# Kernel optimization log

Measured on AMD Instinct MI355X. Metric: run time of the kernel, lower is better.

## Reference

```python
import jax, jax.numpy as jnp
import numpy as np

B, N, S, K = 16, 4, 64, 50        # batch, n_answers, q_len, n_boxes
VD, QD, H = 1024, 768, 512        # v_dim, q_dim, num_hid


def setup_inputs() -> dict:
    key = jax.random.key(0)
    ks = jax.random.split(key, 10)
    inp = {
        "v": jax.random.normal(ks[0], (B, 1, K, VD), dtype=jnp.float32),
        "q": jax.random.normal(ks[1], (B, N, S, 1, QD), dtype=jnp.float32),
        "box_mask": jax.random.randint(ks[2], (B, K), 0, 2, dtype=jnp.int32),
        "tags_attention": jax.random.normal(ks[3], (B, K), dtype=jnp.float32),
        # learned params (nn.Linear stores weight as [out, in])
        "Wv": jax.random.normal(ks[4], (H, VD), dtype=jnp.float32) * 0.02,
        "bv": jnp.zeros((H,), dtype=jnp.float32),
        "Wq": jax.random.normal(ks[5], (H, QD), dtype=jnp.float32) * 0.02,
        "bq": jnp.zeros((H,), dtype=jnp.float32),
        "Wl": jax.random.normal(ks[6], (1, H), dtype=jnp.float32) * 0.02,
        "bl": jnp.zeros((1,), dtype=jnp.float32),
    }
    return inp


def reference(v, q, box_mask, tags_attention, Wv, bv, Wq, bq, Wl, bl):
    # v_proj = Linear(v).unsqueeze(1): [B,1,K,H] -> [B,1,1,K,H]
    v_proj = (jnp.einsum('bokd,hd->bokh', v, Wv) + bv)[:, None]
    # q_proj: [B,N,S,1,H]
    q_proj = jnp.einsum('bnsod,hd->bnsoh', q, Wq) + bq
    # broadcast add + tanh: joint_repr [B,N,S,K,H] (the big intermediate)
    joint_repr = jnp.tanh(v_proj + q_proj)
    # score reduce over H: logits [B,N,S,K]
    logits = jnp.einsum('bnskh,oh->bnsko', joint_repr, Wl)[..., 0] + bl[0]
    # masked softmax over boxes with mask box_mask[:,None,None] -> [B,1,1,K]
    mask = (box_mask > 0)[:, None, None]
    w = jax.nn.softmax(jnp.where(mask, logits, jnp.float32(-1e9)), axis=-1)
    return w
```

## Files before the change

kernel.cpp:

```cpp
#include <hip/hip_runtime.h>
#include <hip/hip_bf16.h>
#include <cstddef>


typedef __attribute__((ext_vector_type(4))) float        f32x4;
typedef __attribute__((ext_vector_type(8))) short        bfrag;
typedef __attribute__((ext_vector_type(4))) unsigned int u32x4;

__device__ __forceinline__ void gload4(const float* g, float* l) {
  __builtin_amdgcn_global_load_lds((const __attribute__((address_space(1))) void*)g,
                                   (__attribute__((address_space(3))) void*)l, 4, 0, 0);
}

__device__ __forceinline__ unsigned int cvtpk(float a, float b) {
  unsigned int r;
  asm("v_cvt_pk_bf16_f32 %0, %1, %2" : "=v"(r) : "v"(a), "v"(b));
  return r;
}

__global__ void __launch_bounds__(256) gemm_fused(
    const float* __restrict__ v,  const float* __restrict__ q,
    const float* __restrict__ Wv, const float* __restrict__ bv,
    const float* __restrict__ Wq, const float* __restrict__ bq,
    float* __restrict__ vpw, float* __restrict__ qpw) {
  __shared__ unsigned short As[2][64 * 64];
  __shared__ unsigned short Bs[2][64 * 64];

  const int id = blockIdx.x;
  const int m  = (id & 7) + ((id >> 6) << 3);
  const int nt = (id >> 3) & 7;
  if (m >= 77) return;

  const int t = threadIdx.x;

  const float* A; const float* W; const float* bias; float* C;
  int M, Kd, m0;
  if (m < 13) { A = v; W = Wv; bias = bv; C = vpw; M = 800;  Kd = 1024; m0 = m * 64; }
  else        { A = q; W = Wq; bias = bq; C = qpw; M = 4096; Kd = 768;  m0 = (m - 13) * 64; }
  const int n0 = nt * 64;

  const int lane = t & 63;
  const int wave = t >> 6;
  const int wm   = wave >> 1;
  const int wn   = wave & 1;
  const int la   = lane & 15;
  const int lb   = lane >> 4;

  const int srow = t >> 2;
  const int skq  = (t & 3) * 16;

  int gr = m0 + srow; if (gr >= M) gr = M - 1;
  const float* Arow = A + (size_t)gr * Kd + skq;
  const float* Wrow = W + (size_t)(n0 + srow) * Kd + skq;

  f32x4 acc[2][2] = {};
  f32x4 raA[4], rbA[4], raB[4], rbB[4];

  auto loadG = [&](f32x4* ra, f32x4* rb, int s) {
    const float* ap = Arow + s * 64;
    const float* wp = Wrow + s * 64;
#pragma unroll
    for (int i = 0; i < 4; ++i) ra[i] = *(const f32x4*)&ap[i * 4];
#pragma unroll
    for (int i = 0; i < 4; ++i) rb[i] = *(const f32x4*)&wp[i * 4];
  };

  const int o0 = (srow * 128 + skq * 2)      ^ ((srow & 7) << 4);
  const int o1 = (srow * 128 + skq * 2 + 16) ^ ((srow & 7) << 4);

  auto writeL = [&](unsigned short* da, unsigned short* db,
                    const f32x4* ra, const f32x4* rb) {
    u32x4 p;
    p[0] = cvtpk(ra[0][0], ra[0][1]); p[1] = cvtpk(ra[0][2], ra[0][3]);
    p[2] = cvtpk(ra[1][0], ra[1][1]); p[3] = cvtpk(ra[1][2], ra[1][3]);
    *(u32x4*)((char*)da + o0) = p;
    p[0] = cvtpk(ra[2][0], ra[2][1]); p[1] = cvtpk(ra[2][2], ra[2][3]);
    p[2] = cvtpk(ra[3][0], ra[3][1]); p[3] = cvtpk(ra[3][2], ra[3][3]);
    *(u32x4*)((char*)da + o1) = p;
    p[0] = cvtpk(rb[0][0], rb[0][1]); p[1] = cvtpk(rb[0][2], rb[0][3]);
    p[2] = cvtpk(rb[1][0], rb[1][1]); p[3] = cvtpk(rb[1][2], rb[1][3]);
    *(u32x4*)((char*)db + o0) = p;
    p[0] = cvtpk(rb[2][0], rb[2][1]); p[1] = cvtpk(rb[2][2], rb[2][3]);
    p[2] = cvtpk(rb[3][0], rb[3][1]); p[3] = cvtpk(rb[3][2], rb[3][3]);
    *(u32x4*)((char*)db + o1) = p;
  };

  auto compute = [&](const unsigned short* sa, const unsigned short* sb) {
    bfrag af[2][2], bf[2][2];
#pragma unroll
    for (int r = 0; r < 2; ++r)
#pragma unroll
      for (int kk = 0; kk < 2; ++kk) {
        int rowa = wm * 32 + r * 16 + la;
        af[r][kk] = *(const bfrag*)((const char*)sa +
                     ((rowa * 128 + kk * 64 + lb * 16) ^ ((rowa & 7) << 4)));
        int rowb = wn * 32 + r * 16 + la;
        bf[r][kk] = *(const bfrag*)((const char*)sb +
                     ((rowb * 128 + kk * 64 + lb * 16) ^ ((rowb & 7) << 4)));
      }
#pragma unroll
    for (int kk = 0; kk < 2; ++kk)
#pragma unroll
      for (int r = 0; r < 2; ++r)
#pragma unroll
        for (int c = 0; c < 2; ++c)
          acc[r][c] = __builtin_amdgcn_mfma_f32_16x16x32_bf16(af[r][kk], bf[c][kk], acc[r][c], 0, 0, 0);
  };

  const int nsteps = Kd >> 6;
  loadG(raA, rbA, 0);
  writeL(As[0], Bs[0], raA, rbA);
  loadG(raB, rbB, 1);
  __syncthreads();
  for (int s = 0; s < nsteps; s += 2) {
    if (s + 2 < nsteps) loadG(raA, rbA, s + 2);
    compute(As[0], Bs[0]);
    writeL(As[1], Bs[1], raB, rbB);
    __syncthreads();
    if (s + 3 < nsteps) loadG(raB, rbB, s + 3);
    compute(As[1], Bs[1]);
    if (s + 2 < nsteps) writeL(As[0], Bs[0], raA, rbA);
    __syncthreads();
  }

  const float CEXP = 2.885390081777927f;
#pragma unroll
  for (int c = 0; c < 2; ++c) {
    int col = n0 + wn * 32 + c * 16 + la;
    float bcol = bias[col];
#pragma unroll
    for (int r = 0; r < 2; ++r) {
      int mbase = m0 + wm * 32 + r * 16 + lb * 4;
#pragma unroll
      for (int e = 0; e < 4; ++e) {
        int mr = mbase + e;
        if (mr < M)
          C[(size_t)mr * 512 + col] =
              __builtin_amdgcn_exp2f((acc[r][c][e] + bcol) * CEXP);
      }
    }
  }
}

__global__ void __launch_bounds__(512) stage3_kernel(
    const float* __restrict__ vp, const float* __restrict__ qp,
    const float* __restrict__ wl, const int* __restrict__ box_mask,
    float* __restrict__ out) {
  __shared__ float vpS[2][50][64];
  __shared__ float qpS[2][8][64];
  __shared__ float wlS[2][64];

  const int b     = blockIdx.y;
  const int chunk = blockIdx.x;
  const int t     = threadIdx.x;
  const int wv    = t >> 6;
  const int k     = t & 63;
  const int rowg  = b * 256 + chunk * 8 + wv;
  const float* qrow = qp + (size_t)rowg * 512;

  const int kc = (k < 50) ? k : k - 14;
  const int cb = kc * 256 + ((kc & 7) << 4);
  const int lsrc = k ^ (wv << 2);

  auto STAGE = [&](int buf, int h0) {
#pragma unroll
    for (int i = 0; i < 7; ++i) {
      int kr = i * 8 + wv;
      if (kr < 50)
        gload4(vp + (size_t)(b * 50 + kr) * 512 + h0 + lsrc, &vpS[buf][kr][0]);
    }
    gload4(qrow + h0 + k, &qpS[buf][wv][0]);
    if (wv == 0) gload4(wl + h0 + k, &wlS[buf][0]);
  };

  float a0 = 0.f, a1 = 0.f, a2 = 0.f, a3 = 0.f;

  STAGE(0, 0);
  __syncthreads();
  int buf = 0;
  for (int c = 0; c < 8; ++c) {
    if (c < 7) STAGE(buf ^ 1, (c + 1) * 64);
    const char* vb = (const char*)&vpS[buf][0][0];
#pragma unroll
    for (int hh = 0; hh < 64; hh += 4) {
      f32x4 v4 = *(const f32x4*)(vb + (cb ^ (hh << 2)));
      f32x4 q4 = *(const f32x4*)&qpS[buf][wv][hh];
      f32x4 w4 = *(const f32x4*)&wlS[buf][hh];
      a0 = fmaf(w4[0], __builtin_amdgcn_rcpf(fmaf(v4[0], q4[0], 1.f)), a0);
      a1 = fmaf(w4[1], __builtin_amdgcn_rcpf(fmaf(v4[1], q4[1], 1.f)), a1);
      a2 = fmaf(w4[2], __builtin_amdgcn_rcpf(fmaf(v4[2], q4[2], 1.f)), a2);
      a3 = fmaf(w4[3], __builtin_amdgcn_rcpf(fmaf(v4[3], q4[3], 1.f)), a3);
    }
    __syncthreads();
    buf ^= 1;
  }

  float logit = -2.f * ((a0 + a1) + (a2 + a3));

  int   msk = (k < 50) ? box_mask[b * 50 + k] : 0;
  float l   = (k < 50 && msk > 0) ? logit : -1e9f;

  float mx = l;
#pragma unroll
  for (int off = 32; off; off >>= 1) mx = fmaxf(mx, __shfl_xor(mx, off));
  float e = (k < 50) ? __builtin_amdgcn_exp2f((l - mx) * 1.4426950408889634f) : 0.f;
  float s = e;
#pragma unroll
  for (int off = 32; off; off >>= 1) s += __shfl_xor(s, off);

  if (k < 50) out[(size_t)rowg * 50 + k] = e / s;
}

extern "C" void kernel_launch(void* const* d_in, const int* in_sizes, int n_in,
                              void* d_out, int out_size, void* d_ws, size_t ws_size,
                              hipStream_t stream) {
  const float* v        = (const float*)d_in[0];
  const float* q        = (const float*)d_in[1];
  const int*   box_mask = (const int*)d_in[2];
  const float* Wv       = (const float*)d_in[4];
  const float* bv       = (const float*)d_in[5];
  const float* Wq       = (const float*)d_in[6];
  const float* bq       = (const float*)d_in[7];
  const float* Wl       = (const float*)d_in[8];
  float* out = (float*)d_out;

  char* ws = (char*)d_ws;
  float* vpw = (float*)(ws);
  float* qpw = (float*)(ws + 1638400);

  gemm_fused<<<dim3(640),   256, 0, stream>>>(v, q, Wv, bv, Wq, bq, vpw, qpw);
  stage3_kernel<<<dim3(32, 16), 512, 0, stream>>>(vpw, qpw, Wl, box_mask, out);
}
```

Baseline: 54.35 us.

## Restructure stage3 to stage whole batch v_proj in LDS and register-accumulate per box

```diff
diff --git a/kernel.cpp b/kernel.cpp
--- a/kernel.cpp
+++ b/kernel.cpp
@@ -3,9 +3,14 @@
 #include <cstddef>
 
 
+typedef __attribute__((ext_vector_type(2))) float        f32x2;
 typedef __attribute__((ext_vector_type(4))) float        f32x4;
 typedef __attribute__((ext_vector_type(8))) short        bfrag;
 typedef __attribute__((ext_vector_type(4))) unsigned int u32x4;
+
+#define LGKM0  asm volatile("s_waitcnt lgkmcnt(0)" ::: "memory")
+#define SBAR   __builtin_amdgcn_s_barrier()
+#define SCHED0 __builtin_amdgcn_sched_barrier(0)
 
 __device__ __forceinline__ void gload4(const float* g, float* l) {
   __builtin_amdgcn_global_load_lds((const __attribute__((address_space(1))) void*)g,
@@ -16,6 +21,12 @@
   unsigned int r;
   asm("v_cvt_pk_bf16_f32 %0, %1, %2" : "=v"(r) : "v"(a), "v"(b));
   return r;
+}
+
+template<int CTRL>
+__device__ __forceinline__ float dpp_add(float x) {
+  int r = __builtin_amdgcn_update_dpp(0, __float_as_int(x), CTRL, 0xF, 0xF, false);
+  return x + __int_as_float(r);
 }
 
 __global__ void __launch_bounds__(256) gemm_fused(
@@ -110,17 +121,23 @@
   const int nsteps = Kd >> 6;
   loadG(raA, rbA, 0);
   writeL(As[0], Bs[0], raA, rbA);
-  loadG(raB, rbB, 1);
-  __syncthreads();
+  loadG(raA, rbA, 1);
+  loadG(raB, rbB, 2);
+  LGKM0; SCHED0; SBAR; SCHED0;
   for (int s = 0; s < nsteps; s += 2) {
-    if (s + 2 < nsteps) loadG(raA, rbA, s + 2);
     compute(As[0], Bs[0]);
-    writeL(As[1], Bs[1], raB, rbB);
-    __syncthreads();
-    if (s + 3 < nsteps) loadG(raB, rbB, s + 3);
+    SBAR; SCHED0;
+    writeL(As[1], Bs[1], raA, rbA);
+    if (s + 3 < nsteps) loadG(raA, rbA, s + 3);
+    LGKM0; SCHED0; SBAR; SCHED0;
     compute(As[1], Bs[1]);
-    if (s + 2 < nsteps) writeL(As[0], Bs[0], raA, rbA);
-    __syncthreads();
+    SBAR; SCHED0;
+    if (s + 2 < nsteps) {
+      writeL(As[0], Bs[0], raB, rbB);
+      if (s + 4 < nsteps) loadG(raB, rbB, s + 4);
+      LGKM0; SCHED0;
+    }
+    SBAR; SCHED0;
   }
 
   const float CEXP = 2.885390081777927f;
@@ -142,60 +159,70 @@
   }
 }
 
-__global__ void __launch_bounds__(512) stage3_kernel(
+__global__ void __launch_bounds__(1024, 4) stage3_kernel(
     const float* __restrict__ vp, const float* __restrict__ qp,
     const float* __restrict__ wl, const int* __restrict__ box_mask,
     float* __restrict__ out) {
-  __shared__ float vpS[2][50][64];
-  __shared__ float qpS[2][8][64];
-  __shared__ float wlS[2][64];
-
-  const int b     = blockIdx.y;
-  const int chunk = blockIdx.x;
-  const int t     = threadIdx.x;
-  const int wv    = t >> 6;
-  const int k     = t & 63;
-  const int rowg  = b * 256 + chunk * 8 + wv;
+  __shared__ float vpS[50][512];
+  __shared__ float redS[16][64][4];
+
+  const int b    = blockIdx.y;
+  const int grp  = blockIdx.x;
+  const int t    = threadIdx.x;
+  const int wv   = t >> 6;
+  const int lane = t & 63;
+  const int rowg = b * 256 + grp * 16 + wv;
+
   const float* qrow = qp + (size_t)rowg * 512;
-
-  const int kc = (k < 50) ? k : k - 14;
-  const int cb = kc * 256 + ((kc & 7) << 4);
-  const int lsrc = k ^ (wv << 2);
-
-  auto STAGE = [&](int buf, int h0) {
-#pragma unroll
-    for (int i = 0; i < 7; ++i) {
-      int kr = i * 8 + wv;
-      if (kr < 50)
-        gload4(vp + (size_t)(b * 50 + kr) * 512 + h0 + lsrc, &vpS[buf][kr][0]);
+  f32x2 eqr[4], wlr[4];
+#pragma unroll
+  for (int j = 0; j < 4; ++j) {
+    eqr[j] = *(const f32x2*)&qrow[j * 128 + 2 * lane];
+    f32x2 w = *(const f32x2*)&wl[j * 128 + 2 * lane];
+    wlr[j][0] = -2.f * w[0];
+    wlr[j][1] = -2.f * w[1];
+  }
+
+  {
+    float* vf = &vpS[0][0];
+    const float* src = vp + (size_t)b * 25600;
+    const int ub = wv * 64;
+#pragma unroll
+    for (int i = 0; i < 25; ++i)
+      gload4(src + i * 1024 + t, vf + i * 1024 + ub);
+  }
+  __syncthreads();
+
+  float acc[50];
+#pragma unroll
+  for (int k = 0; k < 50; ++k) acc[k] = 0.f;
+
+#pragma unroll
+  for (int k = 0; k < 50; ++k) {
+    const f32x2* vr = (const f32x2*)&vpS[k][0];
+#pragma unroll
+    for (int j = 0; j < 4; ++j) {
+      f32x2 v2 = vr[j * 64 + lane];
+      acc[k] = fmaf(wlr[j][0], __builtin_amdgcn_rcpf(fmaf(v2[0], eqr[j][0], 1.f)), acc[k]);
+      acc[k] = fmaf(wlr[j][1], __builtin_amdgcn_rcpf(fmaf(v2[1], eqr[j][1], 1.f)), acc[k]);
     }
-    gload4(qrow + h0 + k, &qpS[buf][wv][0]);
-    if (wv == 0) gload4(wl + h0 + k, &wlS[buf][0]);
-  };
-
-  float a0 = 0.f, a1 = 0.f, a2 = 0.f, a3 = 0.f;
-
-  STAGE(0, 0);
-  __syncthreads();
-  int buf = 0;
-  for (int c = 0; c < 8; ++c) {
-    if (c < 7) STAGE(buf ^ 1, (c + 1) * 64);
-    const char* vb = (const char*)&vpS[buf][0][0];
-#pragma unroll
-    for (int hh = 0; hh < 64; hh += 4) {
-      f32x4 v4 = *(const f32x4*)(vb + (cb ^ (hh << 2)));
-      f32x4 q4 = *(const f32x4*)&qpS[buf][wv][hh];
-      f32x4 w4 = *(const f32x4*)&wlS[buf][hh];
-      a0 = fmaf(w4[0], __builtin_amdgcn_rcpf(fmaf(v4[0], q4[0], 1.f)), a0);
-      a1 = fmaf(w4[1], __builtin_amdgcn_rcpf(fmaf(v4[1], q4[1], 1.f)), a1);
-      a2 = fmaf(w4[2], __builtin_amdgcn_rcpf(fmaf(v4[2], q4[2], 1.f)), a2);
-      a3 = fmaf(w4[3], __builtin_amdgcn_rcpf(fmaf(v4[3], q4[3], 1.f)), a3);
-    }
-    __syncthreads();
-    buf ^= 1;
-  }
-
-  float logit = -2.f * ((a0 + a1) + (a2 + a3));
+  }
+
+  const int g  = lane >> 4;
+  const int li = lane & 15;
+#pragma unroll
+  for (int k = 0; k < 50; ++k) {
+    float s = acc[k];
+    s = dpp_add<0x128>(s);
+    s = dpp_add<0x124>(s);
+    s = dpp_add<0x122>(s);
+    s = dpp_add<0x121>(s);
+    if (li == (k & 15)) redS[wv][k][g] = s;
+  }
+
+  const int k = lane;
+  f32x4 rv = *(const f32x4*)&redS[wv][k][0];
+  float logit = (rv[0] + rv[1]) + (rv[2] + rv[3]);
 
   int   msk = (k < 50) ? box_mask[b * 50 + k] : 0;
   float l   = (k < 50 && msk > 0) ? logit : -1e9f;
@@ -228,6 +255,6 @@
   float* vpw = (float*)(ws);
   float* qpw = (float*)(ws + 1638400);
 
-  gemm_fused<<<dim3(640),   256, 0, stream>>>(v, q, Wv, bv, Wq, bq, vpw, qpw);
-  stage3_kernel<<<dim3(32, 16), 512, 0, stream>>>(vpw, qpw, Wl, box_mask, out);
-}
+  gemm_fused<<<dim3(640),     256,  0, stream>>>(v, q, Wv, bv, Wq, bq, vpw, qpw);
+  stage3_kernel<<<dim3(16, 16), 1024, 0, stream>>>(vpw, qpw, Wl, box_mask, out);
+}
```

New measurement: 171.8 us. 3.16x slower.
